# Performance work log

Hardware: AMD Instinct MI355X
Metric: run time of the kernel (lower is better)

Reference implementation:

```python
import jax, jax.numpy as jnp
import numpy as np

L, N, V = 24, 1024, 50277  # layers, d_model, vocab
F = 4 * N                   # ffn hidden


def _ln(x, w, b):
    mu = jnp.mean(x)
    var = jnp.mean(jnp.square(x - mu))
    return (x - mu) * jax.lax.rsqrt(var + 1e-5) * w + b


def setup_inputs():
    key = jax.random.key(0)
    ks = jax.random.split(key, 24)
    nrm = lambda k, shape, s=0.02: jax.random.normal(k, shape, dtype=jnp.float32) * s
    inp = {}
    inp["ctx"] = jax.random.randint(ks[0], (2,), 0, V, dtype=jnp.int32)
    state = jnp.zeros((5 * L, N), dtype=jnp.float32)
    state = state.at[4::5].set(-1e30)  # pp rows initialized to -1e30 (empty_state)
    inp["state"] = state
    inp["emb"] = nrm(ks[1], (V, N), 1.0)
    inp["ln0_w"] = jnp.ones((N,), jnp.float32)
    inp["ln0_b"] = jnp.zeros((N,), jnp.float32)
    inp["ln1_w"] = jnp.ones((L, N), jnp.float32)
    inp["ln1_b"] = jnp.zeros((L, N), jnp.float32)
    inp["att_mix_k"] = jax.random.uniform(ks[2], (L, N), dtype=jnp.float32)
    inp["att_mix_v"] = jax.random.uniform(ks[3], (L, N), dtype=jnp.float32)
    inp["att_mix_r"] = jax.random.uniform(ks[4], (L, N), dtype=jnp.float32)
    inp["time_first"] = nrm(ks[5], (L, N), 0.5)
    inp["time_decay"] = -jnp.exp(nrm(ks[6], (L, N), 0.5))  # loader applies -exp()
    inp["att_kw"] = nrm(ks[7], (L, N, N))
    inp["att_vw"] = nrm(ks[8], (L, N, N))
    inp["att_rw"] = nrm(ks[9], (L, N, N))
    inp["att_ow"] = nrm(ks[10], (L, N, N))
    inp["ln2_w"] = jnp.ones((L, N), jnp.float32)
    inp["ln2_b"] = jnp.zeros((L, N), jnp.float32)
    inp["ffn_mix_k"] = jax.random.uniform(ks[11], (L, N), dtype=jnp.float32)
    inp["ffn_mix_r"] = jax.random.uniform(ks[12], (L, N), dtype=jnp.float32)
    inp["ffn_kw"] = nrm(ks[13], (L, F, N))
    inp["ffn_vw"] = nrm(ks[14], (L, N, F))
    inp["ffn_rw"] = nrm(ks[15], (L, N, N))
    inp["lnout_w"] = jnp.ones((N,), jnp.float32)
    inp["lnout_b"] = jnp.zeros((N,), jnp.float32)
    inp["head"] = nrm(ks[16], (V, N))
    return inp


def reference(ctx, state, emb, ln0_w, ln0_b, ln1_w, ln1_b, att_mix_k, att_mix_v,
              att_mix_r, time_first, time_decay, att_kw, att_vw, att_rw, att_ow,
              ln2_w, ln2_b, ffn_mix_k, ffn_mix_r, ffn_kw, ffn_vw, ffn_rw,
              lnout_w, lnout_b, head):
    # token embedding mix of the last two tokens (RWKV_RNN.forward)
    x0 = (emb[ctx[-1]] * 4.0 + emb[ctx[-2]]) * 0.2
    x0 = _ln(x0, ln0_w, ln0_b)  # blocks.0.ln0 applied before layer 0
    st = state.reshape(L, 5, N)

    def step(x, per):
        (s, l1w, l1b, amk, amv, amr, tf, td, kw, vw, rw, ow,
         l2w, l2b, fmk, fmr, fkw, fvw, frw) = per
        # --- SA: WKV linear-attention recurrence (single token) ---
        xl = _ln(x, l1w, l1b)
        xk = xl * amk + s[1] * (1 - amk)
        xv = xl * amv + s[1] * (1 - amv)
        xr = xl * amr + s[1] * (1 - amr)
        r = jax.nn.sigmoid(rw @ xr)
        k = kw @ xk
        v = vw @ xv
        aa, bb, pp = s[2], s[3], s[4]
        ww = tf + k
        q = jnp.maximum(pp, ww)
        e1 = jnp.exp(pp - q)
        e2 = jnp.exp(ww - q)
        a = e1 * aa + e2 * v
        b = e1 * bb + e2
        ww2 = pp + td
        q2 = jnp.maximum(ww2, k)
        f1 = jnp.exp(ww2 - q2)
        f2 = jnp.exp(k - q2)
        naa = f1 * aa + f2 * v
        nbb = f1 * bb + f2
        npp = q2
        sx = x + ow @ (r * a / b)
        # --- FF: gated squared-relu channel mixing ---
        x2 = _ln(sx, l2w, l2b)
        fxk = x2 * fmk + s[0] * (1 - fmk)
        fxr = x2 * fmr + s[0] * (1 - fmr)
        r2 = jax.nn.sigmoid(frw @ fxr)
        kk = jnp.square(jax.nn.relu(fkw @ fxk))
        out = sx + r2 * (fvw @ kk)
        ns = jnp.stack([x2, xl, naa, nbb, npp])  # [5, N] new state rows
        return out, ns

    xs = (st, ln1_w, ln1_b, att_mix_k, att_mix_v, att_mix_r, time_first,
          time_decay, att_kw, att_vw, att_rw, att_ow, ln2_w, ln2_b,
          ffn_mix_k, ffn_mix_r, ffn_kw, ffn_vw, ffn_rw)
    xf, new_st = jax.lax.scan(step, x0, xs)
    logits = head @ _ln(xf, lnout_w, lnout_b)
    return logits, new_st.reshape(5 * L, N)
```

## Files before the change

### kernel.cpp

```cpp
#include <hip/hip_runtime.h>
#include <math.h>

#define N 1024
#define F 4096
#define NLAYERS 24
#define VOCAB 50277
#define GRID 256
#define BLOCK 512

#define SXACC_OFF N
#define FACC_OFF (N + 8192)
#define BAR_OFF_BYTES 69632
#define LINE 16
#define BAR_DWORDS (256 * LINE)
#define WS_CLEAR_BYTES (BAR_OFF_BYTES + BAR_DWORDS * 4)

__device__ __forceinline__ float dot4(float4 a, float4 b) {
  return fmaf(a.x, b.x, fmaf(a.y, b.y, fmaf(a.z, b.z, a.w * b.w)));
}
__device__ __forceinline__ float wred(float v) {
#pragma unroll
  for (int o = 32; o > 0; o >>= 1) v += __shfl_down(v, o, 64);
  return v;
}
__device__ __forceinline__ float bfly(float v) {
#pragma unroll
  for (int o = 1; o < 64; o <<= 1) v += __shfl_xor(v, o, 64);
  return v;
}
__device__ __forceinline__ float sigmoidf(float x) { return 1.f / (1.f + expf(-x)); }

__device__ __forceinline__ float2 ld_c2(const float* p) {
  unsigned long long u = __hip_atomic_load((const unsigned long long*)p,
                                           __ATOMIC_RELAXED, __HIP_MEMORY_SCOPE_AGENT);
  float2 f;
  f.x = __uint_as_float((unsigned)u);
  f.y = __uint_as_float((unsigned)(u >> 32));
  return f;
}
__device__ __forceinline__ void st_c(float* p, float v) {
  __hip_atomic_store(p, v, __ATOMIC_RELAXED, __HIP_MEMORY_SCOPE_AGENT);
}
__device__ __forceinline__ unsigned ld_cu(const unsigned* p) {
  return __hip_atomic_load(p, __ATOMIC_RELAXED, __HIP_MEMORY_SCOPE_AGENT);
}
__device__ __forceinline__ void st_cu(unsigned* p, unsigned v) {
  __hip_atomic_store(p, v, __ATOMIC_RELAXED, __HIP_MEMORY_SCOPE_AGENT);
}

__device__ __forceinline__ void lbar() {
  asm volatile("s_waitcnt lgkmcnt(0)" ::: "memory");
  __builtin_amdgcn_s_barrier();
}

__device__ __forceinline__ void gbar_arrive(unsigned* arr, unsigned gen, int blk,
                                            int tid) {
  asm volatile("s_waitcnt vmcnt(0) lgkmcnt(0)" ::: "memory");
  __builtin_amdgcn_s_barrier();
  if (tid == 0) st_cu(arr + blk * LINE, gen);
}
__device__ __forceinline__ void sweep_signal(const unsigned* arr, unsigned gen,
                                             int lane, unsigned* s_gen) {
  for (;;) {
    bool ok = true;
#pragma unroll
    for (int i = 0; i < 4; ++i)
      ok &= (ld_cu(arr + (lane * 4 + i) * LINE) >= gen);
    if (__all(ok)) break;
    __builtin_amdgcn_s_sleep(1);
  }
  __hip_atomic_store(s_gen, gen, __ATOMIC_RELAXED, __HIP_MEMORY_SCOPE_WORKGROUP);
}
__device__ __forceinline__ void lds_wait(const unsigned* s_gen, unsigned gen) {
  while (__hip_atomic_load(s_gen, __ATOMIC_RELAXED, __HIP_MEMORY_SCOPE_WORKGROUP) < gen)
    __builtin_amdgcn_s_sleep(1);
}

__device__ __forceinline__ void ln16(float4* q, const float* __restrict__ w,
                                     const float* __restrict__ b, int lane) {
  float s = 0.f, sq = 0.f;
#pragma unroll
  for (int k = 0; k < 4; ++k) {
    s += q[k].x + q[k].y + q[k].z + q[k].w;
    sq += dot4(q[k], q[k]);
  }
  s = bfly(s);
  sq = bfly(sq);
  float mu = s * (1.f / N);
  float rstd = rsqrtf(sq * (1.f / N) - mu * mu + 1e-5f);
#pragma unroll
  for (int k = 0; k < 4; ++k) {
    float4 w4 = ((const float4*)w)[(k << 6) + lane];
    float4 b4 = ((const float4*)b)[(k << 6) + lane];
    q[k].x = (q[k].x - mu) * rstd * w4.x + b4.x;
    q[k].y = (q[k].y - mu) * rstd * w4.y + b4.y;
    q[k].z = (q[k].z - mu) * rstd * w4.z + b4.z;
    q[k].w = (q[k].w - mu) * rstd * w4.w + b4.w;
  }
}

__device__ __forceinline__ float4 mix4(float4 a, float4 s, float4 m) {
  float4 r;
  r.x = a.x * m.x + s.x * (1.f - m.x);
  r.y = a.y * m.y + s.y * (1.f - m.y);
  r.z = a.z * m.z + s.z * (1.f - m.z);
  r.w = a.w * m.w + s.w * (1.f - m.w);
  return r;
}
// ... 4 lines not shown
  float ww = tf + k;
  float q = fmaxf(pp, ww);
  float e1 = expf(pp - q);
  float e2 = expf(ww - q);
  float a = e1 * aa + e2 * v;
  float b = e1 * bb + e2;
  rab = r * a / b;
  float ww2 = pp + td;
  float q2 = fmaxf(ww2, k);
  float f1 = expf(ww2 - q2);
  float f2 = expf(k - q2);
  naa = f1 * aa + f2 * v;
  nbb = f1 * bb + f2;
  npp = q2;
}

__global__ __launch_bounds__(BLOCK, 1) void k_rwkv(
    const int* __restrict__ ctx, const float* __restrict__ state,
    const float* __restrict__ emb, const float* __restrict__ ln0w,
    const float* __restrict__ ln0b, const float* __restrict__ ln1w,
    const float* __restrict__ ln1b, const float* __restrict__ amk,
    const float* __restrict__ amv, const float* __restrict__ amr,
    const float* __restrict__ tf, const float* __restrict__ td,
    const float* __restrict__ kw, const float* __restrict__ vw,
    const float* __restrict__ rw, const float* __restrict__ ow,
    const float* __restrict__ ln2w, const float* __restrict__ ln2b,
    const float* __restrict__ fmk, const float* __restrict__ fmr,
    const float* __restrict__ fkw, const float* __restrict__ fvw,
    const float* __restrict__ frw, const float* __restrict__ lnoutw,
    const float* __restrict__ lnoutb, const float* __restrict__ head,
    float* __restrict__ out, float* __restrict__ ws, unsigned* __restrict__ bar) {
  __shared__ __align__(16) float s_vx[N];
  __shared__ __align__(16) float s_sx[N];
  __shared__ __align__(16) float s_kk[16];
  __shared__ __align__(16) float s_ex[16];
  __shared__ unsigned s_gen;

  const int tid = threadIdx.x;
  const int lane = tid & 63;
  const int wid = tid >> 6;
  const int blk = blockIdx.x;
  const int i0 = 2 * tid;
  const size_t nn = (size_t)N * N;

  if (tid == 0) s_gen = 0;
  __syncthreads();

  float* logits = out;
  float* st_out = out + VOCAB;
  float* r2buf = ws;
  float* sxacc = ws + SXACC_OFF;
  float* facc = ws + FACC_OFF;
  unsigned genc = 0;

  const int xcd = blk & 7, sgrp = blk >> 3;
  const int jm = sgrp & 3, gg = sgrp >> 2;
  const int tt = xcd + (gg << 3);
  const int c0 = (tt << 4) + (jm << 2);

  const int rowA = c0 + (wid & 3);
  const int gk0 = (blk << 4) + wid, gk1 = gk0 + 8;
  const int rR = (blk << 2) + (wid & 3);
  const int rv0 = (tid + (blk << 2)) & (N - 1);
  const int rv1 = (rv0 + 512) & (N - 1);

  float4 pa0[4], pa1[4], pow0, pow1, pk0[4], pk1[4], pcr[4], pf0[4], pf1[4];

  {
    const float* W0 = ((wid < 4) ? kw : vw) + (size_t)rowA * N;
#pragma unroll
    for (int k = 0; k < 4; ++k) pa0[k] = ((const float4*)W0)[(k << 6) + lane];
    if (wid < 4) {
      const float* W1 = rw + (size_t)rowA * N;
#pragma unroll
      for (int k = 0; k < 4; ++k) pa1[k] = ((const float4*)W1)[(k << 6) + lane];
    }
    pow0 = *(const float4*)(ow + (size_t)rv0 * N + c0);
    pow1 = *(const float4*)(ow + (size_t)rv1 * N + c0);
  }

  for (int l = 0; l < NLAYERS; ++l) {
    const float* st_l = state + (size_t)l * 5 * N;
    float* sto = st_out + (size_t)l * 5 * N;
    const int p = l & 1;

    {
      float kaa = 0.f, kbb = 0.f, kpp = 0.f, ktf = 0.f, ktd = 0.f;
      if (tid < 4) {
        int ii = c0 + tid;
        kaa = st_l[2 * N + ii];
        kbb = st_l[3 * N + ii];
        kpp = st_l[4 * N + ii];
        ktf = tf[l * N + ii];
        ktd = td[l * N + ii];
      }
      if (tid < 16) st_c(sxacc + (1 - p) * 4096 + blk * 16 + tid, 0.f);

      float2 xin;
      if (l == 0) {
        int t1 = ctx[1], t0c = ctx[0];
        float2 e1 = ((const float2*)(emb + (size_t)t1 * N))[tid];
        float2 e0 = ((const float2*)(emb + (size_t)t0c * N))[tid];
        xin.x = (e1.x * 4.f + e0.x) * 0.2f;
        xin.y = (e1.y * 4.f + e0.y) * 0.2f;
      } else {
        float2 r22 = ld_c2(r2buf + i0);
        const float* fb = facc + (1 - p) * 4096;
        float fax = 0.f, fay = 0.f;
#pragma unroll
        for (int c = 0; c < 4; ++c) {
          float2 t2 = ld_c2(fb + c * N + i0);
          fax += t2.x;
          fay += t2.y;
        }
        xin.x = s_sx[i0] + r22.x * fax;
        xin.y = s_sx[i0 + 1] + r22.y * fay;
      }
      ((float2*)s_vx)[tid] = xin;
      lbar();
      float4 xq[4];
#pragma unroll
      for (int k = 0; k < 4; ++k) xq[k] = ((const float4*)s_vx)[(k << 6) + lane];
      if (l == 0) {
        ln16(xq, ln0w, ln0b, lane);
        lbar();
        if (wid == 1) {
#pragma unroll
          for (int k = 0; k < 4; ++k) ((float4*)s_vx)[(k << 6) + lane] = xq[k];
        }
      }
      float4 xl[4];
#pragma unroll
      for (int k = 0; k < 4; ++k) xl[k] = xq[k];
      ln16(xl, ln1w + l * N, ln1b + l * N, lane);
      if (blk == 4 && wid == 1) {
#pragma unroll
        for (int k = 0; k < 4; ++k) ((float4*)(sto + N))[(k << 6) + lane] = xl[k];
      }
      if (wid < 4) {
        float dK = 0.f, dR = 0.f;
#pragma unroll
        for (int k = 0; k < 4; ++k) {
          float4 s1 = ((const float4*)(st_l + N))[(k << 6) + lane];
          float4 mk = mix4(xl[k], s1, ((const float4*)(amk + l * N))[(k << 6) + lane]);
          float4 mr = mix4(xl[k], s1, ((const float4*)(amr + l * N))[(k << 6) + lane]);
          dK += dot4(pa0[k], mk);
          dR += dot4(pa1[k], mr);
        }
        dK = wred(dK);
        dR = wred(dR);
        if (lane == 0) {
          s_ex[wid] = dK;
          s_ex[8 + wid] = sigmoidf(dR);
        }
      } else {
        float dV = 0.f;
#pragma unroll
        for (int k = 0; k < 4; ++k) {
          float4 s1 = ((const float4*)(st_l + N))[(k << 6) + lane];
          float4 mv = mix4(xl[k], s1, ((const float4*)(amv + l * N))[(k << 6) + lane]);
          dV += dot4(pa0[k], mv);
        }
        dV = wred(dV);
        if (lane == 0) s_ex[4 + (wid & 3)] = dV;
      }
      lbar();
      if (tid < 4) {
        float kv = s_ex[tid], vv = s_ex[4 + tid], rr = s_ex[8 + tid];
        float rab, naa, nbb, npp;
        wkv1(kv, vv, rr, kaa, kbb, kpp, ktf, ktd, rab, naa, nbb, npp);
        int ii = c0 + tid;
        sto[2 * N + ii] = naa;
        sto[3 * N + ii] = nbb;
        sto[4 * N + ii] = npp;
        s_ex[12 + tid] = rab;
      }
      lbar();
      float4 rab4 = *((const float4*)(s_ex + 12));
      float* sxa = sxacc + p * 4096 + (blk & 3) * N;
      unsafeAtomicAdd(sxa + rv0, dot4(pow0, rab4));
      unsafeAtomicAdd(sxa + rv1, dot4(pow1, rab4));
    }
    gbar_arrive(bar, ++genc, blk, tid);
    {
      auto pfC = [&]() {
        const float* fkw_l = fkw + (size_t)l * F * N;
#pragma unroll
        for (int k = 0; k < 4; ++k)
          pk0[k] = ((const float4*)(fkw_l + (size_t)gk0 * N))[(k << 6) + lane];
#pragma unroll
        for (int k = 0; k < 4; ++k)
          pk1[k] = ((const float4*)(fkw_l + (size_t)gk1 * N))[(k << 6) + lane];
        if (wid >= 4) {
          const float* WR = frw + l * nn + (size_t)rR * N;
#pragma unroll
          for (int k = 0; k < 4; ++k) pcr[k] = ((const float4*)WR)[(k << 6) + lane];
        }
        const float* fvb = fvw + (size_t)l * N * F + (blk << 4);
#pragma unroll
        for (int i = 0; i < 4; ++i) pf0[i] = ((const float4*)(fvb + (size_t)rv0 * F))[i];
#pragma unroll
        for (int i = 0; i < 4; ++i) pf1[i] = ((const float4*)(fvb + (size_t)rv1 * F))[i];
      };
      if (wid == 0) {
        sweep_signal(bar, genc, lane, &s_gen);
        pfC();
      } else {
        pfC();
        lds_wait(&s_gen, genc);
      }
    }

    {
      if (tid < 16) st_c(facc + (1 - p) * 4096 + blk * 16 + tid, 0.f);
      const float* sb = sxacc + p * 4096;
      float fax = 0.f, fay = 0.f;
#pragma unroll
      for (int c = 0; c < 4; ++c) {
        float2 t2 = ld_c2(sb + c * N + i0);
        fax += t2.x;
        fay += t2.y;
      }
      float2 sx2;
      sx2.x = s_vx[i0] + fax;
      sx2.y = s_vx[i0 + 1] + fay;
      ((float2*)s_sx)[tid] = sx2;
      lbar();
      float4 x2q[4];
#pragma unroll
      for (int k = 0; k < 4; ++k) x2q[k] = ((const float4*)s_sx)[(k << 6) + lane];
      ln16(x2q, ln2w + l * N, ln2b + l * N, lane);
      if (blk == 5 && wid == 1) {
#pragma unroll
        for (int k = 0; k < 4; ++k) ((float4*)sto)[(k << 6) + lane] = x2q[k];
      }
      float4 mk[4];
#pragma unroll
      for (int k = 0; k < 4; ++k) {
        float4 s0 = ((const float4*)st_l)[(k << 6) + lane];
        mk[k] = mix4(x2q[k], s0, ((const float4*)(fmk + l * N))[(k << 6) + lane]);
      }
      float d0 = 0.f, d1 = 0.f;
#pragma unroll
      for (int k = 0; k < 4; ++k) {
        d0 += dot4(pk0[k], mk[k]);
        d1 += dot4(pk1[k], mk[k]);
      }
      d0 = wred(d0);
      d1 = wred(d1);
      if (lane == 0) {
        float t0 = fmaxf(d0, 0.f);
        s_kk[wid] = t0 * t0;
        float t1 = fmaxf(d1, 0.f);
        s_kk[8 + wid] = t1 * t1;
      }
      if (wid >= 4) {
        float dr = 0.f;
#pragma unroll
        for (int k = 0; k < 4; ++k) {
          float4 s0 = ((const float4*)st_l)[(k << 6) + lane];
          float4 mr = mix4(x2q[k], s0, ((const float4*)(fmr + l * N))[(k << 6) + lane]);
          dr += dot4(pcr[k], mr);
        }
        dr = wred(dr);
        if (lane == 0) st_c(r2buf + rR, sigmoidf(dr));
      }
      lbar();
      float4 K0 = ((const float4*)s_kk)[0];
      float4 K1 = ((const float4*)s_kk)[1];
      float4 K2 = ((const float4*)s_kk)[2];
      float4 K3 = ((const float4*)s_kk)[3];
      float* fc = facc + p * 4096 + (blk & 3) * N;
      unsafeAtomicAdd(fc + rv0, dot4(pf0[0], K0) + dot4(pf0[1], K1) +
                                    dot4(pf0[2], K2) + dot4(pf0[3], K3));
      unsafeAtomicAdd(fc + rv1, dot4(pf1[0], K0) + dot4(pf1[1], K1) +
                                    dot4(pf1[2], K2) + dot4(pf1[3], K3));
    }
    gbar_arrive(bar, ++genc, blk, tid);
    {
      auto pfA = [&]() {
        if (l + 1 < NLAYERS) {
          const float* W0 = ((wid < 4) ? kw : vw) + (l + 1) * nn + (size_t)rowA * N;
#pragma unroll
          for (int k = 0; k < 4; ++k) pa0[k] = ((const float4*)W0)[(k << 6) + lane];
          if (wid < 4) {
            const float* W1 = rw + (l + 1) * nn + (size_t)rowA * N;
#pragma unroll
            for (int k = 0; k < 4; ++k) pa1[k] = ((const float4*)W1)[(k << 6) + lane];
          }
          const float* owl = ow + (l + 1) * nn;
          pow0 = *(const float4*)(owl + (size_t)rv0 * N + c0);
          pow1 = *(const float4*)(owl + (size_t)rv1 * N + c0);
        }
      };
      if (wid == 0) {
        sweep_signal(bar, genc, lane, &s_gen);
        pfA();
      } else {
        pfA();
        lds_wait(&s_gen, genc);
      }
    }
  }

  {
    float2 r22 = ld_c2(r2buf + i0);
    const float* fb = facc + ((NLAYERS - 1) & 1) * 4096;
    float fax = 0.f, fay = 0.f;
#pragma unroll
    for (int c = 0; c < 4; ++c) {
      float2 t2 = ld_c2(fb + c * N + i0);
      fax += t2.x;
      fay += t2.y;
    }
    float2 xf2;
    xf2.x = s_sx[i0] + r22.x * fax;
    xf2.y = s_sx[i0 + 1] + r22.y * fay;
    ((float2*)s_vx)[tid] = xf2;
    lbar();
    float4 xf[4];
#pragma unroll
    for (int k = 0; k < 4; ++k) xf[k] = ((const float4*)s_vx)[(k << 6) + lane];
    ln16(xf, lnoutw, lnoutb, lane);
    int gw = (blk << 3) + wid;
    for (int base = gw * 4; base < VOCAB; base += GRID * 8 * 4) {
      float4 h[4][4];
#pragma unroll
      for (int rr = 0; rr < 4; ++rr) {
        int row = base + rr;
        if (row < VOCAB) {
          const float4* hp = (const float4*)(head + (size_t)row * N);
#pragma unroll
          for (int k = 0; k < 4; ++k) h[rr][k] = hp[(k << 6) + lane];
        }
      }
// ... 58 lines not shown
```

Before: 620.7 us.

## Issue weight prefetches before grid-barrier arrive and compute WKV redundantly per thread

Moves the next-phase weight prefetches ahead of the grid-barrier arrive, using counted s_waitcnt vmcnt so only the older stores and atomics must finish before the flag is published. The prefetch loads can then overlap the barrier wait. Every thread also computes the 4-element WKV update redundantly from LDS, which removes one workgroup barrier. The hand-counted vmcnt values are fragile: if the compiler emits a different number of loads, atomics could still be in flight when the flag is published, breaking correctness.

After: 746.1 us. +20.2%, slower.

```diff
diff --git a/kernel.cpp b/kernel.cpp
--- a/kernel.cpp
+++ b/kernel.cpp
@@ -53,9 +53,8 @@
   __builtin_amdgcn_s_barrier();
 }
 
-__device__ __forceinline__ void gbar_arrive(unsigned* arr, unsigned gen, int blk,
+__device__ __forceinline__ void arrive_flag(unsigned* arr, unsigned gen, int blk,
                                             int tid) {
-  asm volatile("s_waitcnt vmcnt(0) lgkmcnt(0)" ::: "memory");
   __builtin_amdgcn_s_barrier();
   if (tid == 0) st_cu(arr + blk * LINE, gen);
 }
@@ -146,6 +145,7 @@
   __shared__ __align__(16) float s_sx[N];
   __shared__ __align__(16) float s_kk[16];
   __shared__ __align__(16) float s_ex[16];
+  __shared__ float s_wkv[20];
   __shared__ unsigned s_gen;
 
   const int tid = threadIdx.x;
@@ -197,14 +197,13 @@
     const int p = l & 1;
 
     {
-      float kaa = 0.f, kbb = 0.f, kpp = 0.f, ktf = 0.f, ktd = 0.f;
       if (tid < 4) {
         int ii = c0 + tid;
-        kaa = st_l[2 * N + ii];
-        kbb = st_l[3 * N + ii];
-        kpp = st_l[4 * N + ii];
-        ktf = tf[l * N + ii];
-        ktd = td[l * N + ii];
+        s_wkv[tid] = st_l[2 * N + ii];
+        s_wkv[4 + tid] = st_l[3 * N + ii];
+        s_wkv[8 + tid] = st_l[4 * N + ii];
+        s_wkv[12 + tid] = tf[l * N + ii];
+        s_wkv[16 + tid] = td[l * N + ii];
       }
       if (tid < 16) st_c(sxacc + (1 - p) * 4096 + blk * 16 + tid, 0.f);
 
@@ -277,51 +276,55 @@
         if (lane == 0) s_ex[4 + (wid & 3)] = dV;
       }
       lbar();
-      if (tid < 4) {
-        float kv = s_ex[tid], vv = s_ex[4 + tid], rr = s_ex[8 + tid];
-        float rab, naa, nbb, npp;
-        wkv1(kv, vv, rr, kaa, kbb, kpp, ktf, ktd, rab, naa, nbb, npp);
-        int ii = c0 + tid;
-        sto[2 * N + ii] = naa;
-        sto[3 * N + ii] = nbb;
-        sto[4 * N + ii] = npp;
-        s_ex[12 + tid] = rab;
-      }
-      lbar();
-      float4 rab4 = *((const float4*)(s_ex + 12));
+      float rab_[4], naa_[4], nbb_[4], npp_[4];
+#pragma unroll
+      for (int j = 0; j < 4; ++j) {
+        wkv1(s_ex[j], s_ex[4 + j], s_ex[8 + j], s_wkv[j], s_wkv[4 + j],
+             s_wkv[8 + j], s_wkv[12 + j], s_wkv[16 + j], rab_[j], naa_[j],
+             nbb_[j], npp_[j]);
+      }
+      if (tid == 0) {
+#pragma unroll
+        for (int j = 0; j < 4; ++j) {
+          int ii = c0 + j;
+          sto[2 * N + ii] = naa_[j];
+          sto[3 * N + ii] = nbb_[j];
+          sto[4 * N + ii] = npp_[j];
+        }
+      }
+      float4 rab4 = make_float4(rab_[0], rab_[1], rab_[2], rab_[3]);
       float* sxa = sxacc + p * 4096 + (blk & 3) * N;
       unsafeAtomicAdd(sxa + rv0, dot4(pow0, rab4));
       unsafeAtomicAdd(sxa + rv1, dot4(pow1, rab4));
     }
-    gbar_arrive(bar, ++genc, blk, tid);
+    __builtin_amdgcn_sched_barrier(0);
     {
-      auto pfC = [&]() {
-        const float* fkw_l = fkw + (size_t)l * F * N;
-#pragma unroll
-        for (int k = 0; k < 4; ++k)
-          pk0[k] = ((const float4*)(fkw_l + (size_t)gk0 * N))[(k << 6) + lane];
-#pragma unroll
-        for (int k = 0; k < 4; ++k)
-          pk1[k] = ((const float4*)(fkw_l + (size_t)gk1 * N))[(k << 6) + lane];
-        if (wid >= 4) {
-          const float* WR = frw + l * nn + (size_t)rR * N;
-#pragma unroll
-          for (int k = 0; k < 4; ++k) pcr[k] = ((const float4*)WR)[(k << 6) + lane];
-        }
-        const float* fvb = fvw + (size_t)l * N * F + (blk << 4);
-#pragma unroll
-        for (int i = 0; i < 4; ++i) pf0[i] = ((const float4*)(fvb + (size_t)rv0 * F))[i];
-#pragma unroll
-        for (int i = 0; i < 4; ++i) pf1[i] = ((const float4*)(fvb + (size_t)rv1 * F))[i];
-      };
-      if (wid == 0) {
-        sweep_signal(bar, genc, lane, &s_gen);
-        pfC();
-      } else {
-        pfC();
-        lds_wait(&s_gen, genc);
-      }
-    }
+      const float* fkw_l = fkw + (size_t)l * F * N;
+#pragma unroll
+      for (int k = 0; k < 4; ++k)
+        pk0[k] = ((const float4*)(fkw_l + (size_t)gk0 * N))[(k << 6) + lane];
+#pragma unroll
+      for (int k = 0; k < 4; ++k)
+        pk1[k] = ((const float4*)(fkw_l + (size_t)gk1 * N))[(k << 6) + lane];
+      if (wid >= 4) {
+        const float* WR = frw + l * nn + (size_t)rR * N;
+#pragma unroll
+        for (int k = 0; k < 4; ++k) pcr[k] = ((const float4*)WR)[(k << 6) + lane];
+      }
+      const float* fvb = fvw + (size_t)l * N * F + (blk << 4);
+#pragma unroll
+      for (int i = 0; i < 4; ++i) pf0[i] = ((const float4*)(fvb + (size_t)rv0 * F))[i];
+#pragma unroll
+      for (int i = 0; i < 4; ++i) pf1[i] = ((const float4*)(fvb + (size_t)rv1 * F))[i];
+    }
+    __builtin_amdgcn_sched_barrier(0);
+    if (wid < 4)
+      asm volatile("s_waitcnt vmcnt(16) lgkmcnt(0)" ::: "memory");
+    else
+      asm volatile("s_waitcnt vmcnt(20) lgkmcnt(0)" ::: "memory");
+    arrive_flag(bar, ++genc, blk, tid);
+    if (wid == 0) sweep_signal(bar, genc, lane, &s_gen);
+    else lds_wait(&s_gen, genc);
 
     {
       if (tid < 16) st_c(facc + (1 - p) * 4096 + blk * 16 + tid, 0.f);
@@ -388,31 +391,30 @@
       unsafeAtomicAdd(fc + rv1, dot4(pf1[0], K0) + dot4(pf1[1], K1) +
                                     dot4(pf1[2], K2) + dot4(pf1[3], K3));
     }
-    gbar_arrive(bar, ++genc, blk, tid);
-    {
-      auto pfA = [&]() {
-        if (l + 1 < NLAYERS) {
-          const float* W0 = ((wid < 4) ? kw : vw) + (l + 1) * nn + (size_t)rowA * N;
-#pragma unroll
-          for (int k = 0; k < 4; ++k) pa0[k] = ((const float4*)W0)[(k << 6) + lane];
-          if (wid < 4) {
-            const float* W1 = rw + (l + 1) * nn + (size_t)rowA * N;
-#pragma unroll
-            for (int k = 0; k < 4; ++k) pa1[k] = ((const float4*)W1)[(k << 6) + lane];
-          }
-          const float* owl = ow + (l + 1) * nn;
-          pow0 = *(const float4*)(owl + (size_t)rv0 * N + c0);
-          pow1 = *(const float4*)(owl + (size_t)rv1 * N + c0);
-        }
-      };
-      if (wid == 0) {
-        sweep_signal(bar, genc, lane, &s_gen);
-        pfA();
-      } else {
-        pfA();
-        lds_wait(&s_gen, genc);
-      }
-    }
+    __builtin_amdgcn_sched_barrier(0);
+    if (l + 1 < NLAYERS) {
+      const float* W0 = ((wid < 4) ? kw : vw) + (l + 1) * nn + (size_t)rowA * N;
+#pragma unroll
+      for (int k = 0; k < 4; ++k) pa0[k] = ((const float4*)W0)[(k << 6) + lane];
+      if (wid < 4) {
+        const float* W1 = rw + (l + 1) * nn + (size_t)rowA * N;
+#pragma unroll
+        for (int k = 0; k < 4; ++k) pa1[k] = ((const float4*)W1)[(k << 6) + lane];
+      }
+      const float* owl = ow + (l + 1) * nn;
+      pow0 = *(const float4*)(owl + (size_t)rv0 * N + c0);
+      pow1 = *(const float4*)(owl + (size_t)rv1 * N + c0);
+      __builtin_amdgcn_sched_barrier(0);
+      if (wid < 4)
+        asm volatile("s_waitcnt vmcnt(10) lgkmcnt(0)" ::: "memory");
+      else
+        asm volatile("s_waitcnt vmcnt(6) lgkmcnt(0)" ::: "memory");
+    } else {
+      asm volatile("s_waitcnt vmcnt(0) lgkmcnt(0)" ::: "memory");
+    }
+    arrive_flag(bar, ++genc, blk, tid);
+    if (wid == 0) sweep_signal(bar, genc, lane, &s_gen);
+    else lds_wait(&s_gen, genc);
   }
 
   {
```

## Dedicate wave 0 to barrier polling and issue weight prefetch before arriving

Applied to the files above, without the earlier changes.

Wave 0 no longer takes part in the matvec rows. It only polls the grid barrier and loads the small ow/fvw slices, and the attention and FFN weight rows are spread over the remaining seven waves. Worker waves now issue their next-phase weight prefetch before arriving at the grid barrier. They use partial vmcnt waits so the arrival does not block on those in-flight loads. This aims to overlap weight streaming with barrier latency. The cost is an uneven row split across waves and fragile hand-counted waitcnt values.

After: 989.3 us. +59.4%, slower.

```diff
diff --git a/kernel.cpp b/kernel.cpp
--- a/kernel.cpp
+++ b/kernel.cpp
@@ -14,6 +14,8 @@
 #define LINE 16
 #define BAR_DWORDS (256 * LINE)
 #define WS_CLEAR_BYTES (BAR_OFF_BYTES + BAR_DWORDS * 4)
+
+#define DRAIN(K) asm volatile("s_waitcnt vmcnt(" #K ") lgkmcnt(0)" ::: "memory")
 
 __device__ __forceinline__ float dot4(float4 a, float4 b) {
   return fmaf(a.x, b.x, fmaf(a.y, b.y, fmaf(a.z, b.z, a.w * b.w)));
@@ -53,9 +55,8 @@
   __builtin_amdgcn_s_barrier();
 }
 
-__device__ __forceinline__ void gbar_arrive(unsigned* arr, unsigned gen, int blk,
+__device__ __forceinline__ void arrive_flag(unsigned* arr, unsigned gen, int blk,
                                             int tid) {
-  asm volatile("s_waitcnt vmcnt(0) lgkmcnt(0)" ::: "memory");
   __builtin_amdgcn_s_barrier();
   if (tid == 0) st_cu(arr + blk * LINE, gen);
 }
@@ -69,11 +70,12 @@
     if (__all(ok)) break;
     __builtin_amdgcn_s_sleep(1);
   }
-  __hip_atomic_store(s_gen, gen, __ATOMIC_RELAXED, __HIP_MEMORY_SCOPE_WORKGROUP);
+  __hip_atomic_store(s_gen, gen, __ATOMIC_RELEASE, __HIP_MEMORY_SCOPE_WORKGROUP);
 }
 __device__ __forceinline__ void lds_wait(const unsigned* s_gen, unsigned gen) {
-  while (__hip_atomic_load(s_gen, __ATOMIC_RELAXED, __HIP_MEMORY_SCOPE_WORKGROUP) < gen)
+  while (__hip_atomic_load(s_gen, __ATOMIC_ACQUIRE, __HIP_MEMORY_SCOPE_WORKGROUP) < gen)
     __builtin_amdgcn_s_sleep(1);
+  asm volatile("" ::: "memory");
 }
 
 __device__ __forceinline__ void ln16(float4* q, const float* __restrict__ w,
@@ -144,13 +146,14 @@
     float* __restrict__ out, float* __restrict__ ws, unsigned* __restrict__ bar) {
   __shared__ __align__(16) float s_vx[N];
   __shared__ __align__(16) float s_sx[N];
+  __shared__ __align__(16) float s_ex[16];
   __shared__ __align__(16) float s_kk[16];
-  __shared__ __align__(16) float s_ex[16];
   __shared__ unsigned s_gen;
 
   const int tid = threadIdx.x;
   const int lane = tid & 63;
   const int wid = tid >> 6;
+  const bool work = (wid > 0);
   const int blk = blockIdx.x;
   const int i0 = 2 * tid;
   const size_t nn = (size_t)N * N;
@@ -167,29 +170,77 @@
 
   const int xcd = blk & 7, sgrp = blk >> 3;
   const int jm = sgrp & 3, gg = sgrp >> 2;
-  const int tt = xcd + (gg << 3);
-  const int c0 = (tt << 4) + (jm << 2);
-
-  const int rowA = c0 + (wid & 3);
-  const int gk0 = (blk << 4) + wid, gk1 = gk0 + 8;
-  const int rR = (blk << 2) + (wid & 3);
-  const int rv0 = (tid + (blk << 2)) & (N - 1);
-  const int rv1 = (rv0 + 512) & (N - 1);
-
-  float4 pa0[4], pa1[4], pow0, pow1, pk0[4], pk1[4], pcr[4], pf0[4], pf1[4];
-
-  {
-    const float* W0 = ((wid < 4) ? kw : vw) + (size_t)rowA * N;
-#pragma unroll
-    for (int k = 0; k < 4; ++k) pa0[k] = ((const float4*)W0)[(k << 6) + lane];
-    if (wid < 4) {
-      const float* W1 = rw + (size_t)rowA * N;
-#pragma unroll
-      for (int k = 0; k < 4; ++k) pa1[k] = ((const float4*)W1)[(k << 6) + lane];
-    }
-    pow0 = *(const float4*)(ow + (size_t)rv0 * N + c0);
-    pow1 = *(const float4*)(ow + (size_t)rv1 * N + c0);
-  }
+  const int c0 = (((xcd + (gg << 3)) << 4) + (jm << 2));
+
+  const int wl = (wid - 1) * 64 + lane;
+  const int rI = wid - 1, rJ = wid + 6;
+  const bool hasJ = (wid >= 1 && wid <= 5);
+  const int iA = (wid <= 6) ? 3 * (wid - 1) : 18;
+  const int iB = iA + 1;
+  const int iC = iA + 2;
+  const bool hasC = (wid >= 1 && wid <= 6);
+  const int rv0 = work ? ((wl + (blk << 2)) & (N - 1)) : ((896 + lane + (blk << 2)) & (N - 1));
+  const int rv1 = work ? ((wl + 448 + (blk << 2)) & (N - 1)) : ((960 + lane + (blk << 2)) & (N - 1));
+
+  float4 paI[4], paJ[4], powr0, powr1;
+  float4 pkA[4], pkB[4], pkC[4], pf0[4], pf1[4];
+  float kaa = 0.f, kbb = 0.f, kpp = 0.f, ktf = 0.f, ktd = 0.f;
+
+  auto parow = [&](int r, int lc) -> const float* {
+    int m = r >> 2;
+    const float* base = (m == 0) ? kw : (m == 1) ? vw : rw;
+    return base + (size_t)lc * nn + (size_t)(c0 + (r & 3)) * N;
+  };
+  auto pcrow = [&](int i, int lc) -> const float* {
+    return (i < 16) ? fkw + (size_t)lc * F * N + (size_t)((blk << 4) + i) * N
+                    : frw + (size_t)lc * nn + (size_t)((blk << 2) + (i - 16)) * N;
+  };
+  auto pfA_rows = [&](int lc) {
+    const float* WI = parow(rI, lc);
+#pragma unroll
+    for (int k = 0; k < 4; ++k) paI[k] = ((const float4*)WI)[(k << 6) + lane];
+    if (hasJ) {
+      const float* WJ = parow(rJ, lc);
+#pragma unroll
+      for (int k = 0; k < 4; ++k) paJ[k] = ((const float4*)WJ)[(k << 6) + lane];
+    }
+    const float* owl = ow + (size_t)lc * nn;
+    powr0 = *(const float4*)(owl + (size_t)rv0 * N + c0);
+    powr1 = *(const float4*)(owl + (size_t)rv1 * N + c0);
+  };
+  auto pfC_rows = [&](int lc) {
+    const float* WA = pcrow(iA, lc);
+#pragma unroll
+    for (int k = 0; k < 4; ++k) pkA[k] = ((const float4*)WA)[(k << 6) + lane];
+    const float* WB = pcrow(iB, lc);
+#pragma unroll
+    for (int k = 0; k < 4; ++k) pkB[k] = ((const float4*)WB)[(k << 6) + lane];
+    if (hasC) {
+      const float* WC = pcrow(iC, lc);
+#pragma unroll
+      for (int k = 0; k < 4; ++k) pkC[k] = ((const float4*)WC)[(k << 6) + lane];
+    }
+    const float* fvb = fvw + (size_t)lc * N * F + (blk << 4);
+#pragma unroll
+    for (int i = 0; i < 4; ++i) pf0[i] = ((const float4*)(fvb + (size_t)rv0 * F))[i];
+#pragma unroll
+    for (int i = 0; i < 4; ++i) pf1[i] = ((const float4*)(fvb + (size_t)rv1 * F))[i];
+  };
+  auto pfA_w0 = [&](int lc) {
+    const float* owl = ow + (size_t)lc * nn;
+    powr0 = *(const float4*)(owl + (size_t)rv0 * N + c0);
+    powr1 = *(const float4*)(owl + (size_t)rv1 * N + c0);
+  };
+  auto pfC_w0 = [&](int lc) {
+    const float* fvb = fvw + (size_t)lc * N * F + (blk << 4);
+#pragma unroll
+    for (int i = 0; i < 4; ++i) pf0[i] = ((const float4*)(fvb + (size_t)rv0 * F))[i];
+#pragma unroll
+    for (int i = 0; i < 4; ++i) pf1[i] = ((const float4*)(fvb + (size_t)rv1 * F))[i];
+  };
+
+  if (work) pfA_rows(0);
+  else pfA_w0(0);
 
   for (int l = 0; l < NLAYERS; ++l) {
     const float* st_l = state + (size_t)l * 5 * N;
@@ -197,7 +248,6 @@
     const int p = l & 1;
 
     {
-      float kaa = 0.f, kbb = 0.f, kpp = 0.f, ktf = 0.f, ktd = 0.f;
       if (tid < 4) {
         int ii = c0 + tid;
         kaa = st_l[2 * N + ii];
@@ -231,56 +281,55 @@
       ((float2*)s_vx)[tid] = xin;
       lbar();
       float4 xq[4];
-#pragma unroll
-      for (int k = 0; k < 4; ++k) xq[k] = ((const float4*)s_vx)[(k << 6) + lane];
+      if (work) {
+#pragma unroll
+        for (int k = 0; k < 4; ++k) xq[k] = ((const float4*)s_vx)[(k << 6) + lane];
+      }
       if (l == 0) {
-        ln16(xq, ln0w, ln0b, lane);
+        if (work) ln16(xq, ln0w, ln0b, lane);
         lbar();
         if (wid == 1) {
 #pragma unroll
           for (int k = 0; k < 4; ++k) ((float4*)s_vx)[(k << 6) + lane] = xq[k];
         }
       }
-      float4 xl[4];
-#pragma unroll
-      for (int k = 0; k < 4; ++k) xl[k] = xq[k];
-      ln16(xl, ln1w + l * N, ln1b + l * N, lane);
-      if (blk == 4 && wid == 1) {
-#pragma unroll
-        for (int k = 0; k < 4; ++k) ((float4*)(sto + N))[(k << 6) + lane] = xl[k];
-      }
-      if (wid < 4) {
-        float dK = 0.f, dR = 0.f;
+      if (work) {
+        float4 xl[4];
+#pragma unroll
+        for (int k = 0; k < 4; ++k) xl[k] = xq[k];
+        ln16(xl, ln1w + l * N, ln1b + l * N, lane);
+        if (blk == 4 && wid == 1) {
+#pragma unroll
+          for (int k = 0; k < 4; ++k) ((float4*)(sto + N))[(k << 6) + lane] = xl[k];
+        }
+        int mI = rI >> 2;
+        float dI = 0.f, dJ = 0.f;
 #pragma unroll
         for (int k = 0; k < 4; ++k) {
           float4 s1 = ((const float4*)(st_l + N))[(k << 6) + lane];
           float4 mk = mix4(xl[k], s1, ((const float4*)(amk + l * N))[(k << 6) + lane]);
+          float4 mv = mix4(xl[k], s1, ((const float4*)(amv + l * N))[(k << 6) + lane]);
           float4 mr = mix4(xl[k], s1, ((const float4*)(amr + l * N))[(k << 6) + lane]);
-          dK += dot4(pa0[k], mk);
-          dR += dot4(pa1[k], mr);
-        }
-        dK = wred(dK);
-        dR = wred(dR);
-        if (lane == 0) {
-          s_ex[wid] = dK;
-          s_ex[8 + wid] = sigmoidf(dR);
-        }
-      } else {
-        float dV = 0.f;
-#pragma unroll
-        for (int k = 0; k < 4; ++k) {
-          float4 s1 = ((const float4*)(st_l + N))[(k << 6) + lane];
-          float4 mv = mix4(xl[k], s1, ((const float4*)(amv + l * N))[(k << 6) + lane]);
-          dV += dot4(pa0[k], mv);
-        }
-        dV = wred(dV);
-        if (lane == 0) s_ex[4 + (wid & 3)] = dV;
+          float4 mmI = (mI == 0) ? mk : ((mI == 1) ? mv : mr);
+          dI += dot4(paI[k], mmI);
+          if (hasJ) {
+            int mJ = rJ >> 2;
+            float4 mmJ = (mJ == 1) ? mv : mr;
+            dJ += dot4(paJ[k], mmJ);
+          }
+        }
+        dI = wred(dI);
+        if (lane == 0) s_ex[rI] = (rI >= 8) ? sigmoidf(dI) : dI;
+        if (hasJ) {
+          dJ = wred(dJ);
+          if (lane == 0) s_ex[rJ] = (rJ >= 8) ? sigmoidf(dJ) : dJ;
+        }
       }
       lbar();
       if (tid < 4) {
-        float kv = s_ex[tid], vv = s_ex[4 + tid], rr = s_ex[8 + tid];
         float rab, naa, nbb, npp;
-        wkv1(kv, vv, rr, kaa, kbb, kpp, ktf, ktd, rab, naa, nbb, npp);
+        wkv1(s_ex[tid], s_ex[4 + tid], s_ex[8 + tid], kaa, kbb, kpp, ktf, ktd,
+             rab, naa, nbb, npp);
         int ii = c0 + tid;
         sto[2 * N + ii] = naa;
         sto[3 * N + ii] = nbb;
@@ -288,39 +337,28 @@
         s_ex[12 + tid] = rab;
       }
       lbar();
-      float4 rab4 = *((const float4*)(s_ex + 12));
-      float* sxa = sxacc + p * 4096 + (blk & 3) * N;
-      unsafeAtomicAdd(sxa + rv0, dot4(pow0, rab4));
-      unsafeAtomicAdd(sxa + rv1, dot4(pow1, rab4));
-    }
-    gbar_arrive(bar, ++genc, blk, tid);
-    {
-      auto pfC = [&]() {
-        const float* fkw_l = fkw + (size_t)l * F * N;
-#pragma unroll
-        for (int k = 0; k < 4; ++k)
-          pk0[k] = ((const float4*)(fkw_l + (size_t)gk0 * N))[(k << 6) + lane];
-#pragma unroll
-        for (int k = 0; k < 4; ++k)
-          pk1[k] = ((const float4*)(fkw_l + (size_t)gk1 * N))[(k << 6) + lane];
-        if (wid >= 4) {
-          const float* WR = frw + l * nn + (size_t)rR * N;
-#pragma unroll
-          for (int k = 0; k < 4; ++k) pcr[k] = ((const float4*)WR)[(k << 6) + lane];
-        }
-        const float* fvb = fvw + (size_t)l * N * F + (blk << 4);
-#pragma unroll
-        for (int i = 0; i < 4; ++i) pf0[i] = ((const float4*)(fvb + (size_t)rv0 * F))[i];
-#pragma unroll
-        for (int i = 0; i < 4; ++i) pf1[i] = ((const float4*)(fvb + (size_t)rv1 * F))[i];
-      };
-      if (wid == 0) {
-        sweep_signal(bar, genc, lane, &s_gen);
-        pfC();
-      } else {
-        pfC();
-        lds_wait(&s_gen, genc);
-      }
+      {
+        float4 rab4 = *((const float4*)(s_ex + 12));
+        float* sxa = sxacc + p * 4096 + (blk & 3) * N;
+        unsafeAtomicAdd(sxa + rv0, dot4(powr0, rab4));
+        unsafeAtomicAdd(sxa + rv1, dot4(powr1, rab4));
+      }
+    }
+    __builtin_amdgcn_sched_barrier(0);
+    if (work) {
+      pfC_rows(l);
+      __builtin_amdgcn_sched_barrier(0);
+      if (wid <= 6) DRAIN(20);
+      else DRAIN(16);
+    } else {
+      DRAIN(0);
+    }
+    arrive_flag(bar, ++genc, blk, tid);
+    if (!work) {
+      sweep_signal(bar, genc, lane, &s_gen);
+      pfC_w0(l);
+    } else {
+      lds_wait(&s_gen, genc);
     }
 
     {
@@ -338,80 +376,68 @@
       sx2.y = s_vx[i0 + 1] + fay;
       ((float2*)s_sx)[tid] = sx2;
       lbar();
-      float4 x2q[4];
-#pragma unroll
-      for (int k = 0; k < 4; ++k) x2q[k] = ((const float4*)s_sx)[(k << 6) + lane];
-      ln16(x2q, ln2w + l * N, ln2b + l * N, lane);
-      if (blk == 5 && wid == 1) {
-#pragma unroll
-        for (int k = 0; k < 4; ++k) ((float4*)sto)[(k << 6) + lane] = x2q[k];
-      }
-      float4 mk[4];
-#pragma unroll
-      for (int k = 0; k < 4; ++k) {
-        float4 s0 = ((const float4*)st_l)[(k << 6) + lane];
-        mk[k] = mix4(x2q[k], s0, ((const float4*)(fmk + l * N))[(k << 6) + lane]);
-      }
-      float d0 = 0.f, d1 = 0.f;
-#pragma unroll
-      for (int k = 0; k < 4; ++k) {
-        d0 += dot4(pk0[k], mk[k]);
-        d1 += dot4(pk1[k], mk[k]);
-      }
-      d0 = wred(d0);
-      d1 = wred(d1);
-      if (lane == 0) {
-        float t0 = fmaxf(d0, 0.f);
-        s_kk[wid] = t0 * t0;
-        float t1 = fmaxf(d1, 0.f);
-        s_kk[8 + wid] = t1 * t1;
-      }
-      if (wid >= 4) {
-        float dr = 0.f;
+      if (work) {
+        float4 x2q[4];
+#pragma unroll
+        for (int k = 0; k < 4; ++k) x2q[k] = ((const float4*)s_sx)[(k << 6) + lane];
+        ln16(x2q, ln2w + l * N, ln2b + l * N, lane);
+        if (blk == 5 && wid == 1) {
+#pragma unroll
+          for (int k = 0; k < 4; ++k) ((float4*)sto)[(k << 6) + lane] = x2q[k];
+        }
+        float dA = 0.f, dB = 0.f, dC = 0.f;
 #pragma unroll
         for (int k = 0; k < 4; ++k) {
           float4 s0 = ((const float4*)st_l)[(k << 6) + lane];
+          float4 mk = mix4(x2q[k], s0, ((const float4*)(fmk + l * N))[(k << 6) + lane]);
           float4 mr = mix4(x2q[k], s0, ((const float4*)(fmr + l * N))[(k << 6) + lane]);
-          dr += dot4(pcr[k], mr);
-        }
-        dr = wred(dr);
-        if (lane == 0) st_c(r2buf + rR, sigmoidf(dr));
+          dA += dot4(pkA[k], (iA < 16) ? mk : mr);
+          dB += dot4(pkB[k], (iB < 16) ? mk : mr);
+          if (hasC) dC += dot4(pkC[k], (iC < 16) ? mk : mr);
+        }
+        dA = wred(dA);
+        dB = wred(dB);
+        if (hasC) dC = wred(dC);
+        if (lane == 0) {
+          if (iA < 16) { float t = fmaxf(dA, 0.f); s_kk[iA] = t * t; }
+          else st_c(r2buf + (blk << 2) + (iA - 16), sigmoidf(dA));
+          if (iB < 16) { float t = fmaxf(dB, 0.f); s_kk[iB] = t * t; }
+          else st_c(r2buf + (blk << 2) + (iB - 16), sigmoidf(dB));
+          if (hasC) {
+            if (iC < 16) { float t = fmaxf(dC, 0.f); s_kk[iC] = t * t; }
+            else st_c(r2buf + (blk << 2) + (iC - 16), sigmoidf(dC));
+          }
+        }
       }
       lbar();
-      float4 K0 = ((const float4*)s_kk)[0];
-      float4 K1 = ((const float4*)s_kk)[1];
-      float4 K2 = ((const float4*)s_kk)[2];
-      float4 K3 = ((const float4*)s_kk)[3];
-      float* fc = facc + p * 4096 + (blk & 3) * N;
-      unsafeAtomicAdd(fc + rv0, dot4(pf0[0], K0) + dot4(pf0[1], K1) +
-                                    dot4(pf0[2], K2) + dot4(pf0[3], K3));
-      unsafeAtomicAdd(fc + rv1, dot4(pf1[0], K0) + dot4(pf1[1], K1) +
-                                    dot4(pf1[2], K2) + dot4(pf1[3], K3));
-    }
-    gbar_arrive(bar, ++genc, blk, tid);
-    {
-      auto pfA = [&]() {
-        if (l + 1 < NLAYERS) {
-          const float* W0 = ((wid < 4) ? kw : vw) + (l + 1) * nn + (size_t)rowA * N;
-#pragma unroll
-          for (int k = 0; k < 4; ++k) pa0[k] = ((const float4*)W0)[(k << 6) + lane];
-          if (wid < 4) {
-            const float* W1 = rw + (l + 1) * nn + (size_t)rowA * N;
-#pragma unroll
-            for (int k = 0; k < 4; ++k) pa1[k] = ((const float4*)W1)[(k << 6) + lane];
-          }
-          const float* owl = ow + (l + 1) * nn;
-          pow0 = *(const float4*)(owl + (size_t)rv0 * N + c0);
-          pow1 = *(const float4*)(owl + (size_t)rv1 * N + c0);
-        }
-      };
-      if (wid == 0) {
-        sweep_signal(bar, genc, lane, &s_gen);
-        pfA();
-      } else {
-        pfA();
-        lds_wait(&s_gen, genc);
-      }
+      {
+        float4 K0 = ((const float4*)s_kk)[0];
+        float4 K1 = ((const float4*)s_kk)[1];
+        float4 K2 = ((const float4*)s_kk)[2];
+        float4 K3 = ((const float4*)s_kk)[3];
+        float* fc = facc + p * 4096 + (blk & 3) * N;
+        unsafeAtomicAdd(fc + rv0, dot4(pf0[0], K0) + dot4(pf0[1], K1) +
+                                      dot4(pf0[2], K2) + dot4(pf0[3], K3));
+        unsafeAtomicAdd(fc + rv1, dot4(pf1[0], K0) + dot4(pf1[1], K1) +
+                                      dot4(pf1[2], K2) + dot4(pf1[3], K3));
+      }
+    }
+    const bool ldav = (l + 1 < NLAYERS);
+    __builtin_amdgcn_sched_barrier(0);
+    if (work && ldav) {
+      pfA_rows(l + 1);
+      __builtin_amdgcn_sched_barrier(0);
+      if (wid <= 5) DRAIN(10);
+      else DRAIN(6);
+    } else {
+      DRAIN(0);
+    }
+    arrive_flag(bar, ++genc, blk, tid);
+    if (!work) {
+      sweep_signal(bar, genc, lane, &s_gen);
+      if (ldav) pfA_w0(l + 1);
+    } else {
+      lds_wait(&s_gen, genc);
     }
   }
 
```

## Offload matvec row work from barrier-polling wave 0 to the other seven waves

Applied to the files above, without the earlier changes.

Wave 0 of each block, which polls the grid barrier, no longer computes any attention or FFN-key dot products. Its rows are redistributed across waves 1-7 with role tables, so some waves take a third row or both K and R rows. Wave 0 only prefetches the ow and fvw column slices, which lets the barrier sweep overlap the other waves' compute. The LDS flag store and load are upgraded to release/acquire to keep ordering intact. The cost is uneven per-wave work and more branches and registers in the worker waves.

Measured after the change: 677.2 us. +9.1%, slower.

```diff
diff --git a/kernel.cpp b/kernel.cpp
--- a/kernel.cpp
+++ b/kernel.cpp
@@ -69,11 +69,12 @@
     if (__all(ok)) break;
     __builtin_amdgcn_s_sleep(1);
   }
-  __hip_atomic_store(s_gen, gen, __ATOMIC_RELAXED, __HIP_MEMORY_SCOPE_WORKGROUP);
+  __hip_atomic_store(s_gen, gen, __ATOMIC_RELEASE, __HIP_MEMORY_SCOPE_WORKGROUP);
 }
 __device__ __forceinline__ void lds_wait(const unsigned* s_gen, unsigned gen) {
-  while (__hip_atomic_load(s_gen, __ATOMIC_RELAXED, __HIP_MEMORY_SCOPE_WORKGROUP) < gen)
+  while (__hip_atomic_load(s_gen, __ATOMIC_ACQUIRE, __HIP_MEMORY_SCOPE_WORKGROUP) < gen)
     __builtin_amdgcn_s_sleep(1);
+  asm volatile("" ::: "memory");
 }
 
 __device__ __forceinline__ void ln16(float4* q, const float* __restrict__ w,
@@ -151,6 +152,7 @@
   const int tid = threadIdx.x;
   const int lane = tid & 63;
   const int wid = tid >> 6;
+  const bool work = (wid > 0);
   const int blk = blockIdx.x;
   const int i0 = 2 * tid;
   const size_t nn = (size_t)N * N;
@@ -170,26 +172,78 @@
   const int tt = xcd + (gg << 3);
   const int c0 = (tt << 4) + (jm << 2);
 
-  const int rowA = c0 + (wid & 3);
+  const bool lo = (wid >= 1 && wid <= 3);
+  const int rowI = lo ? (c0 + wid) : (c0 + (wid & 3));
+  const int exI = lo ? wid : (4 + (wid & 3));
+  const bool hasJ = (wid >= 1 && wid <= 5);
+  const int rowJ = lo ? (c0 + wid) : c0;
+  const int exJ = lo ? (8 + wid) : ((wid == 4) ? 0 : 8);
+  const int mixJ = (wid == 4) ? 0 : 2;
+  const bool needK = lo || (wid == 4);
+  const bool needV = (wid >= 4);
+  const bool needR = lo || (wid == 5);
   const int gk0 = (blk << 4) + wid, gk1 = gk0 + 8;
+  const bool c3k = (wid == 1 || wid == 2);
+  const int gk2 = (blk << 4) + ((wid == 1) ? 0 : 8);
+  const bool c3r = (wid >= 4);
   const int rR = (blk << 2) + (wid & 3);
   const int rv0 = (tid + (blk << 2)) & (N - 1);
   const int rv1 = (rv0 + 512) & (N - 1);
 
   float4 pa0[4], pa1[4], pow0, pow1, pk0[4], pk1[4], pcr[4], pf0[4], pf1[4];
 
-  {
-    const float* W0 = ((wid < 4) ? kw : vw) + (size_t)rowA * N;
+  auto pfA_rows = [&](int lc) {
+    const float* W0 = (lo ? kw : vw) + (size_t)lc * nn + (size_t)rowI * N;
 #pragma unroll
     for (int k = 0; k < 4; ++k) pa0[k] = ((const float4*)W0)[(k << 6) + lane];
-    if (wid < 4) {
-      const float* W1 = rw + (size_t)rowA * N;
+    if (hasJ) {
+      const float* W1 = (lo ? rw : ((wid == 4) ? kw : rw)) + (size_t)lc * nn +
+                        (size_t)rowJ * N;
 #pragma unroll
       for (int k = 0; k < 4; ++k) pa1[k] = ((const float4*)W1)[(k << 6) + lane];
     }
-    pow0 = *(const float4*)(ow + (size_t)rv0 * N + c0);
-    pow1 = *(const float4*)(ow + (size_t)rv1 * N + c0);
-  }
+    const float* owl = ow + (size_t)lc * nn;
+    pow0 = *(const float4*)(owl + (size_t)rv0 * N + c0);
+    pow1 = *(const float4*)(owl + (size_t)rv1 * N + c0);
+  };
+  auto pfA_w0 = [&](int lc) {
+    const float* owl = ow + (size_t)lc * nn;
+    pow0 = *(const float4*)(owl + (size_t)rv0 * N + c0);
+    pow1 = *(const float4*)(owl + (size_t)rv1 * N + c0);
+  };
+  auto pfC_rows = [&](int lc) {
+    const float* fkw_l = fkw + (size_t)lc * F * N;
+#pragma unroll
+    for (int k = 0; k < 4; ++k)
+      pk0[k] = ((const float4*)(fkw_l + (size_t)gk0 * N))[(k << 6) + lane];
+#pragma unroll
+    for (int k = 0; k < 4; ++k)
+      pk1[k] = ((const float4*)(fkw_l + (size_t)gk1 * N))[(k << 6) + lane];
+    if (c3k) {
+#pragma unroll
+      for (int k = 0; k < 4; ++k)
+        pcr[k] = ((const float4*)(fkw_l + (size_t)gk2 * N))[(k << 6) + lane];
+    } else if (c3r) {
+      const float* WR = frw + (size_t)lc * nn + (size_t)rR * N;
+#pragma unroll
+      for (int k = 0; k < 4; ++k) pcr[k] = ((const float4*)WR)[(k << 6) + lane];
+    }
+    const float* fvb = fvw + (size_t)lc * N * F + (blk << 4);
+#pragma unroll
+    for (int i = 0; i < 4; ++i) pf0[i] = ((const float4*)(fvb + (size_t)rv0 * F))[i];
+#pragma unroll
+    for (int i = 0; i < 4; ++i) pf1[i] = ((const float4*)(fvb + (size_t)rv1 * F))[i];
+  };
+  auto pfC_w0 = [&](int lc) {
+    const float* fvb = fvw + (size_t)lc * N * F + (blk << 4);
+#pragma unroll
+    for (int i = 0; i < 4; ++i) pf0[i] = ((const float4*)(fvb + (size_t)rv0 * F))[i];
+#pragma unroll
+    for (int i = 0; i < 4; ++i) pf1[i] = ((const float4*)(fvb + (size_t)rv1 * F))[i];
+  };
+
+  if (work) pfA_rows(0);
+  else pfA_w0(0);
 
   for (int l = 0; l < NLAYERS; ++l) {
     const float* st_l = state + (size_t)l * 5 * N;
@@ -231,56 +285,54 @@
       ((float2*)s_vx)[tid] = xin;
       lbar();
       float4 xq[4];
-#pragma unroll
-      for (int k = 0; k < 4; ++k) xq[k] = ((const float4*)s_vx)[(k << 6) + lane];
+      if (work) {
+#pragma unroll
+        for (int k = 0; k < 4; ++k) xq[k] = ((const float4*)s_vx)[(k << 6) + lane];
+      }
       if (l == 0) {
-        ln16(xq, ln0w, ln0b, lane);
+        if (work) ln16(xq, ln0w, ln0b, lane);
         lbar();
         if (wid == 1) {
 #pragma unroll
           for (int k = 0; k < 4; ++k) ((float4*)s_vx)[(k << 6) + lane] = xq[k];
         }
       }
-      float4 xl[4];
-#pragma unroll
-      for (int k = 0; k < 4; ++k) xl[k] = xq[k];
-      ln16(xl, ln1w + l * N, ln1b + l * N, lane);
-      if (blk == 4 && wid == 1) {
-#pragma unroll
-        for (int k = 0; k < 4; ++k) ((float4*)(sto + N))[(k << 6) + lane] = xl[k];
-      }
-      if (wid < 4) {
-        float dK = 0.f, dR = 0.f;
+      if (work) {
+        float4 xl[4];
+#pragma unroll
+        for (int k = 0; k < 4; ++k) xl[k] = xq[k];
+        ln16(xl, ln1w + l * N, ln1b + l * N, lane);
+        if (blk == 4 && wid == 1) {
+#pragma unroll
+          for (int k = 0; k < 4; ++k) ((float4*)(sto + N))[(k << 6) + lane] = xl[k];
+        }
+        float dI = 0.f, dJ = 0.f;
 #pragma unroll
         for (int k = 0; k < 4; ++k) {
           float4 s1 = ((const float4*)(st_l + N))[(k << 6) + lane];
-          float4 mk = mix4(xl[k], s1, ((const float4*)(amk + l * N))[(k << 6) + lane]);
-          float4 mr = mix4(xl[k], s1, ((const float4*)(amr + l * N))[(k << 6) + lane]);
-          dK += dot4(pa0[k], mk);
-          dR += dot4(pa1[k], mr);
-        }
-        dK = wred(dK);
-        dR = wred(dR);
-        if (lane == 0) {
-          s_ex[wid] = dK;
-          s_ex[8 + wid] = sigmoidf(dR);
-        }
-      } else {
-        float dV = 0.f;
-#pragma unroll
-        for (int k = 0; k < 4; ++k) {
-          float4 s1 = ((const float4*)(st_l + N))[(k << 6) + lane];
-          float4 mv = mix4(xl[k], s1, ((const float4*)(amv + l * N))[(k << 6) + lane]);
-          dV += dot4(pa0[k], mv);
-        }
-        dV = wred(dV);
-        if (lane == 0) s_ex[4 + (wid & 3)] = dV;
+          float4 mk, mv, mr;
+          if (needK) mk = mix4(xl[k], s1, ((const float4*)(amk + l * N))[(k << 6) + lane]);
+          if (needV) mv = mix4(xl[k], s1, ((const float4*)(amv + l * N))[(k << 6) + lane]);
+          if (needR) mr = mix4(xl[k], s1, ((const float4*)(amr + l * N))[(k << 6) + lane]);
+          float4 mmI = lo ? mk : mv;
+          dI += dot4(pa0[k], mmI);
+          if (hasJ) {
+            float4 mmJ = (mixJ == 0) ? mk : mr;
+            dJ += dot4(pa1[k], mmJ);
+          }
+        }
+        dI = wred(dI);
+        if (lane == 0) s_ex[exI] = dI;
+        if (hasJ) {
+          dJ = wred(dJ);
+          if (lane == 0) s_ex[exJ] = (exJ >= 8) ? sigmoidf(dJ) : dJ;
+        }
       }
       lbar();
       if (tid < 4) {
-        float kv = s_ex[tid], vv = s_ex[4 + tid], rr = s_ex[8 + tid];
         float rab, naa, nbb, npp;
-        wkv1(kv, vv, rr, kaa, kbb, kpp, ktf, ktd, rab, naa, nbb, npp);
+        wkv1(s_ex[tid], s_ex[4 + tid], s_ex[8 + tid], kaa, kbb, kpp, ktf, ktd,
+             rab, naa, nbb, npp);
         int ii = c0 + tid;
         sto[2 * N + ii] = naa;
         sto[3 * N + ii] = nbb;
@@ -294,33 +346,12 @@
       unsafeAtomicAdd(sxa + rv1, dot4(pow1, rab4));
     }
     gbar_arrive(bar, ++genc, blk, tid);
-    {
-      auto pfC = [&]() {
-        const float* fkw_l = fkw + (size_t)l * F * N;
-#pragma unroll
-        for (int k = 0; k < 4; ++k)
-          pk0[k] = ((const float4*)(fkw_l + (size_t)gk0 * N))[(k << 6) + lane];
-#pragma unroll
-        for (int k = 0; k < 4; ++k)
-          pk1[k] = ((const float4*)(fkw_l + (size_t)gk1 * N))[(k << 6) + lane];
-        if (wid >= 4) {
-          const float* WR = frw + l * nn + (size_t)rR * N;
-#pragma unroll
-          for (int k = 0; k < 4; ++k) pcr[k] = ((const float4*)WR)[(k << 6) + lane];
-        }
-        const float* fvb = fvw + (size_t)l * N * F + (blk << 4);
-#pragma unroll
-        for (int i = 0; i < 4; ++i) pf0[i] = ((const float4*)(fvb + (size_t)rv0 * F))[i];
-#pragma unroll
-        for (int i = 0; i < 4; ++i) pf1[i] = ((const float4*)(fvb + (size_t)rv1 * F))[i];
-      };
-      if (wid == 0) {
-        sweep_signal(bar, genc, lane, &s_gen);
-        pfC();
-      } else {
-        pfC();
-        lds_wait(&s_gen, genc);
-      }
+    if (wid == 0) {
+      sweep_signal(bar, genc, lane, &s_gen);
+      pfC_w0(l);
+    } else {
+      pfC_rows(l);
+      lds_wait(&s_gen, genc);
     }
 
     {
@@ -338,44 +369,44 @@
       sx2.y = s_vx[i0 + 1] + fay;
       ((float2*)s_sx)[tid] = sx2;
       lbar();
-      float4 x2q[4];
-#pragma unroll
-      for (int k = 0; k < 4; ++k) x2q[k] = ((const float4*)s_sx)[(k << 6) + lane];
-      ln16(x2q, ln2w + l * N, ln2b + l * N, lane);
-      if (blk == 5 && wid == 1) {
-#pragma unroll
-        for (int k = 0; k < 4; ++k) ((float4*)sto)[(k << 6) + lane] = x2q[k];
-      }
-      float4 mk[4];
-#pragma unroll
-      for (int k = 0; k < 4; ++k) {
-        float4 s0 = ((const float4*)st_l)[(k << 6) + lane];
-        mk[k] = mix4(x2q[k], s0, ((const float4*)(fmk + l * N))[(k << 6) + lane]);
-      }
-      float d0 = 0.f, d1 = 0.f;
-#pragma unroll
-      for (int k = 0; k < 4; ++k) {
-        d0 += dot4(pk0[k], mk[k]);
-        d1 += dot4(pk1[k], mk[k]);
-      }
-      d0 = wred(d0);
-      d1 = wred(d1);
-      if (lane == 0) {
-        float t0 = fmaxf(d0, 0.f);
-        s_kk[wid] = t0 * t0;
-        float t1 = fmaxf(d1, 0.f);
-        s_kk[8 + wid] = t1 * t1;
-      }
-      if (wid >= 4) {
-        float dr = 0.f;
+      if (work) {
+        float4 x2q[4];
+#pragma unroll
+        for (int k = 0; k < 4; ++k) x2q[k] = ((const float4*)s_sx)[(k << 6) + lane];
+        ln16(x2q, ln2w + l * N, ln2b + l * N, lane);
+        if (blk == 5 && wid == 1) {
+#pragma unroll
+          for (int k = 0; k < 4; ++k) ((float4*)sto)[(k << 6) + lane] = x2q[k];
+        }
+        float d0 = 0.f, d1 = 0.f, d2 = 0.f;
 #pragma unroll
         for (int k = 0; k < 4; ++k) {
           float4 s0 = ((const float4*)st_l)[(k << 6) + lane];
-          float4 mr = mix4(x2q[k], s0, ((const float4*)(fmr + l * N))[(k << 6) + lane]);
-          dr += dot4(pcr[k], mr);
-        }
-        dr = wred(dr);
-        if (lane == 0) st_c(r2buf + rR, sigmoidf(dr));
+          float4 mk = mix4(x2q[k], s0, ((const float4*)(fmk + l * N))[(k << 6) + lane]);
+          d0 += dot4(pk0[k], mk);
+          d1 += dot4(pk1[k], mk);
+          if (c3k) {
+            d2 += dot4(pcr[k], mk);
+          } else if (c3r) {
+            float4 mr = mix4(x2q[k], s0, ((const float4*)(fmr + l * N))[(k << 6) + lane]);
+            d2 += dot4(pcr[k], mr);
+          }
+        }
+        d0 = wred(d0);
+        d1 = wred(d1);
+        if (c3k || c3r) d2 = wred(d2);
+        if (lane == 0) {
+          float t0 = fmaxf(d0, 0.f);
+          s_kk[wid] = t0 * t0;
+          float t1 = fmaxf(d1, 0.f);
+          s_kk[8 + wid] = t1 * t1;
+          if (c3k) {
+            float t2v = fmaxf(d2, 0.f);
+            s_kk[(wid == 1) ? 0 : 8] = t2v * t2v;
+          } else if (c3r) {
+            st_c(r2buf + rR, sigmoidf(d2));
+          }
+        }
       }
       lbar();
       float4 K0 = ((const float4*)s_kk)[0];
@@ -390,26 +421,12 @@
     }
     gbar_arrive(bar, ++genc, blk, tid);
     {
-      auto pfA = [&]() {
-        if (l + 1 < NLAYERS) {
-          const float* W0 = ((wid < 4) ? kw : vw) + (l + 1) * nn + (size_t)rowA * N;
-#pragma unroll
-          for (int k = 0; k < 4; ++k) pa0[k] = ((const float4*)W0)[(k << 6) + lane];
-          if (wid < 4) {
-            const float* W1 = rw + (l + 1) * nn + (size_t)rowA * N;
-#pragma unroll
-            for (int k = 0; k < 4; ++k) pa1[k] = ((const float4*)W1)[(k << 6) + lane];
-          }
-          const float* owl = ow + (l + 1) * nn;
-          pow0 = *(const float4*)(owl + (size_t)rv0 * N + c0);
-          pow1 = *(const float4*)(owl + (size_t)rv1 * N + c0);
-        }
-      };
+      const bool ldav = (l + 1 < NLAYERS);
       if (wid == 0) {
         sweep_signal(bar, genc, lane, &s_gen);
-        pfA();
+        if (ldav) pfA_w0(l + 1);
       } else {
-        pfA();
+        if (ldav) pfA_rows(l + 1);
         lds_wait(&s_gen, genc);
       }
     }
```
